# Kernel optimization log

Hardware: AMD Instinct MI355X
Metric: run time of the kernel (lower is better)

Reference implementation:

```python
import jax, jax.numpy as jnp
import numpy as np

B, HH, WW, DENC = 32, 14, 14, 256
E, H, V, A, T = 512, 512, 30000, 256, 20


def setup_inputs() -> dict:
    key = jax.random.key(0)
    ks = jax.random.split(key, 16)
    s = 0.02
    return {
        "encoder_out": jax.random.normal(ks[0], (B, HH, WW, DENC), jnp.float32),
        "captions": jax.random.randint(ks[1], (B, T), 0, V),
        # Attention params (stored [in, out])
        "W_enc_att": jax.random.normal(ks[2], (DENC, A), jnp.float32) * s,
        "b_enc_att": jnp.zeros((A,), jnp.float32),
        "W_dec_att": jax.random.normal(ks[3], (H, A), jnp.float32) * s,
        "b_dec_att": jnp.zeros((A,), jnp.float32),
        "W_full": jax.random.normal(ks[4], (A, 1), jnp.float32) * s,
        "b_full": jnp.zeros((1,), jnp.float32),
        # Embedding table
        "emb": jax.random.normal(ks[5], (V, E), jnp.float32) * s,
        # LSTMCell params, torch gate order (i, f, g, o) stacked on out dim
        "W_ih": jax.random.normal(ks[6], (E + DENC, 4 * H), jnp.float32) * s,
        "b_ih": jnp.zeros((4 * H,), jnp.float32),
        "W_hh": jax.random.normal(ks[7], (H, 4 * H), jnp.float32) * s,
        "b_hh": jnp.zeros((4 * H,), jnp.float32),
        # Output projection
        "W_fc": jax.random.normal(ks[8], (H, V), jnp.float32) * s,
        "b_fc": jnp.zeros((V,), jnp.float32),
    }


def reference(encoder_out, captions, W_enc_att, b_enc_att, W_dec_att, b_dec_att,
              W_full, b_full, emb, W_ih, b_ih, W_hh, b_hh, W_fc, b_fc):
    # Flatten spatial dims: [B, P, DENC], P = HH*WW
    enc = encoder_out.reshape(encoder_out.shape[0], -1, encoder_out.shape[-1])
    # att1 is constant across timesteps (same math as recomputing each step)
    att1 = enc @ W_enc_att + b_enc_att            # [B, P, A]
    embeddings = emb[captions]                    # [B, T, E]
    x_seq = jnp.swapaxes(embeddings, 0, 1)        # [T, B, E]

    h0 = jnp.zeros((enc.shape[0], H), enc.dtype)
    c0 = jnp.zeros((enc.shape[0], H), enc.dtype)

    def step(carry, x_t):
        h, c = carry
        # Additive attention
        att2 = h @ W_dec_att + b_dec_att                          # [B, A]
        e = (jnp.tanh(att1 + att2[:, None, :]) @ W_full + b_full)[..., 0]  # [B, P]
        alpha = jax.nn.softmax(e, axis=1)                         # [B, P]
        context = jnp.einsum('bp,bpd->bd', alpha, enc)            # [B, DENC]
        # LSTMCell
        x = jnp.concatenate([x_t, context], axis=1)               # [B, E+DENC]
        gates = x @ W_ih + b_ih + h @ W_hh + b_hh                 # [B, 4H]
        i, f, g, o = jnp.split(gates, 4, axis=1)
        c_new = jax.nn.sigmoid(f) * c + jax.nn.sigmoid(i) * jnp.tanh(g)
        h_new = jax.nn.sigmoid(o) * jnp.tanh(c_new)
        # Dropout is identity in eval mode
        out = h_new @ W_fc + b_fc                                 # [B, V]
        return (h_new, c_new), out

    _, outs = jax.lax.scan(step, (h0, c0), x_seq)                 # [T, B, V]
    return jnp.swapaxes(outs, 0, 1)                               # [B, T, V]
```

## Files before the change

kernel.cpp:

```cpp
#include <hip/hip_runtime.h>
#include <hip/hip_bf16.h>
#include <cstddef>

#define BB 32
#define PP 196
#define DENC 256
#define EE 512
#define HH 512
#define AA 256
#define VV 30000
#define TT 20
#define BH (BB*HH)
#define G4 (4*HH)
#define VPAD 30080

typedef __attribute__((ext_vector_type(8))) short short8;
typedef __attribute__((ext_vector_type(4))) float f32x4;

__device__ __forceinline__ float fast_sigmoid(float x) {
    return 1.f / (1.f + __expf(-x));
}
__device__ __forceinline__ float fast_tanh(float x) {
    x = fminf(fmaxf(x, -15.f), 15.f);
    float e = __expf(2.f * x);
    return (e - 1.f) / (e + 1.f);
}
__device__ __forceinline__ void split_bf16(float x, unsigned short& hi, unsigned short& lo) {
    const unsigned u = __float_as_uint(x);
    hi = (unsigned short)(u >> 16);
    const float r = x - __uint_as_float(u & 0xffff0000u);
    lo = (unsigned short)(__float_as_uint(r) >> 16);
}

__global__ void att1_kernel(const float* __restrict__ enc,
                            const float* __restrict__ W,
                            const float* __restrict__ bias,
                            float* __restrict__ att1) {
    __shared__ float xs[8][DENC];
    const int tid = threadIdx.x;
    const int r0 = blockIdx.x * 8;
    #pragma unroll
    for (int bi = 0; bi < 8; ++bi)
        xs[bi][tid] = enc[(size_t)(r0 + bi) * DENC + tid];
    __syncthreads();
    float acc[8];
    const float bv = bias[tid];
    #pragma unroll
    for (int bi = 0; bi < 8; ++bi) acc[bi] = bv;
    #pragma unroll 8
    for (int k = 0; k < DENC; ++k) {
        const float w = W[k * AA + tid];
        #pragma unroll
        for (int bi = 0; bi < 8; ++bi) acc[bi] += xs[bi][k] * w;
    }
    #pragma unroll
    for (int bi = 0; bi < 8; ++bi)
        att1[(size_t)(r0 + bi) * AA + tid] = acc[bi];
}

__global__ void epre_kernel(const int* __restrict__ captions,
                            const float* __restrict__ emb,
                            const float* __restrict__ Wih,
                            const float* __restrict__ bih,
                            const float* __restrict__ bhh,
                            float* __restrict__ Epre) {
    __shared__ float xs[8][EE];
    const int tid = threadIdx.x;
    const int jc = blockIdx.x;
    const int mg = blockIdx.y;
    const int j = jc * 256 + tid;

    #pragma unroll
    for (int i = 0; i < 8; ++i) {
        const int m = mg * 8 + i;
        const int t = m >> 5, b = m & 31;
        const int cap = captions[b * TT + t];
        const float* erow = emb + (size_t)cap * EE;
        xs[i][tid]       = erow[tid];
        xs[i][tid + 256] = erow[tid + 256];
    }
    __syncthreads();

    float acc[8];
    const float bv = bih[j] + bhh[j];
    #pragma unroll
    for (int i = 0; i < 8; ++i) acc[i] = bv;
    #pragma unroll 8
    for (int k = 0; k < EE; ++k) {
        const float w = Wih[(size_t)k * G4 + j];
        #pragma unroll
        for (int i = 0; i < 8; ++i) acc[i] += xs[i][k] * w;
    }
    #pragma unroll
    for (int i = 0; i < 8; ++i)
        Epre[(size_t)(mg * 8 + i) * G4 + j] = acc[i];
}

__global__ __launch_bounds__(1024) void attn_step_kernel(
        int t,
        const float* __restrict__ att1,
        const float* __restrict__ enc,
        float* __restrict__ Hall,
        float* __restrict__ cbuf,
        const float* __restrict__ gates,
        float* __restrict__ context,
        const float* __restrict__ Wda,
        const float* __restrict__ bda,
        const float* __restrict__ Wfull,
        const float* __restrict__ bfull) {
    __shared__ float h_s[HH];
    __shared__ float part[4][256];
    __shared__ float att2_s[AA];
    __shared__ float e_s[256];
    __shared__ float red_s[256];
    const int b = blockIdx.x;
    const int tid = threadIdx.x;

    if (tid < 512) {
        if (t == 0) {
            h_s[tid] = 0.f;
            cbuf[b * HH + tid] = 0.f;
        } else {
            const float* g = gates + b * G4;
            const float gi = g[tid];
            const float gf = g[HH + tid];
            const float gg = g[2 * HH + tid];
            const float go = g[3 * HH + tid];
            const float cp = cbuf[b * HH + tid];
            const float cn = fast_sigmoid(gf) * cp + fast_sigmoid(gi) * fast_tanh(gg);
            const float hn = fast_sigmoid(go) * fast_tanh(cn);
            cbuf[b * HH + tid] = cn;
            Hall[(size_t)(t - 1) * BH + b * HH + tid] = hn;
            h_s[tid] = hn;
        }
    }
    __syncthreads();

    {
        const int q = tid >> 8, col = tid & 255;
        const float* W = Wda + (size_t)(q * 128) * AA + col;
        const float* hh = h_s + q * 128;
        float acc = 0.f;
        #pragma unroll 16
        for (int k = 0; k < 128; ++k) acc += hh[k] * W[(size_t)k * AA];
        part[q][col] = acc;
    }
    __syncthreads();
    if (tid < 256)
        att2_s[tid] = part[0][tid] + part[1][tid] + part[2][tid] + part[3][tid] + bda[tid];
    __syncthreads();

    {
        const int wave = tid >> 6, lane = tid & 63;
        const float bf0 = bfull[0];
        for (int p = wave; p < PP; p += 16) {
            const float* row = att1 + ((size_t)b * PP + p) * AA;
            float s = 0.f;
            #pragma unroll
            for (int q = 0; q < 4; ++q) {
                const int a = lane + q * 64;
                s += fast_tanh(row[a] + att2_s[a]) * Wfull[a];
            }
            #pragma unroll
            for (int off = 32; off > 0; off >>= 1) s += __shfl_down(s, off, 64);
            if (lane == 0) e_s[p] = s + bf0;
        }
    }
    __syncthreads();

    const float val = (tid < PP) ? e_s[tid] : -3.4e38f;
    if (tid < 256) red_s[tid] = val;
    __syncthreads();
    #pragma unroll
    for (int s = 128; s > 0; s >>= 1) {
        if (tid < s) red_s[tid] = fmaxf(red_s[tid], red_s[tid + s]);
        __syncthreads();
    }
    const float mx = red_s[0];
    __syncthreads();
    const float ex = (tid < PP) ? __expf(val - mx) : 0.f;
    if (tid < 256) red_s[tid] = ex;
    __syncthreads();
    #pragma unroll
    for (int s = 128; s > 0; s >>= 1) {
        if (tid < s) red_s[tid] += red_s[tid + s];
        __syncthreads();
    }
    const float inv = 1.f / red_s[0];
    __syncthreads();
    if (tid < 256) e_s[tid] = ex * inv;
    __syncthreads();

    {
        const int q = tid >> 8, col = tid & 255;
        const float* erow = enc + (size_t)b * PP * DENC + col;
        float acc = 0.f;
        const int p0 = q * 49;
        #pragma unroll 7
        for (int p = p0; p < p0 + 49; ++p) acc += e_s[p] * erow[(size_t)p * DENC];
        part[q][col] = acc;
    }
    __syncthreads();
    if (tid < 256)
        context[b * DENC + tid] = part[0][tid] + part[1][tid] + part[2][tid] + part[3][tid];
}

__global__ __launch_bounds__(1024) void gates_kernel(
        int t,
        const float* __restrict__ context,
        const float* __restrict__ Hall,
        const float* __restrict__ Epre,
        const float* __restrict__ Wih,
        const float* __restrict__ Whh,
        float* __restrict__ gates) {
    __shared__ float xs[4][768];
    __shared__ float part[4][256];
    const int tid = threadIdx.x;
    const int jc = blockIdx.x;
    const int bg = blockIdx.y;

    for (int idx = tid; idx < 4 * 768; idx += 1024) {
        const int bi = idx / 768;
        const int k = idx - bi * 768;
        const int b = bg * 4 + bi;
        float v;
        if (k < 256) v = context[b * DENC + k];
        else v = (t > 0) ? Hall[(size_t)(t - 1) * BH + b * HH + (k - 256)] : 0.f;
        xs[bi][k] = v;
    }
    __syncthreads();

    const int kq = tid >> 8;
    const int r = tid & 255;
    const int jl = r & 63, bl = r >> 6;
    const int j = jc * 64 + jl;
    const float* xrow = xs[bl];

    float acc = 0.f;
    if (kq == 0) {
        const float* W1 = Wih + (size_t)512 * G4 + j;
        #pragma unroll 16
        for (int k = 0; k < 192; ++k) acc += xrow[k] * W1[(size_t)k * G4];
    } else if (kq == 1) {
        const float* W1 = Wih + (size_t)704 * G4 + j;
        #pragma unroll 16
        for (int k = 0; k < 64; ++k) acc += xrow[192 + k] * W1[(size_t)k * G4];
        const float* W2 = Whh + j;
        #pragma unroll 16
        for (int k = 0; k < 128; ++k) acc += xrow[256 + k] * W2[(size_t)k * G4];
    } else if (kq == 2) {
        const float* W2 = Whh + (size_t)128 * G4 + j;
        #pragma unroll 16
        for (int k = 0; k < 192; ++k) acc += xrow[384 + k] * W2[(size_t)k * G4];
    } else {
        const float* W2 = Whh + (size_t)320 * G4 + j;
        #pragma unroll 16
        for (int k = 0; k < 192; ++k) acc += xrow[576 + k] * W2[(size_t)k * G4];
    }
    part[kq][r] = acc;
    __syncthreads();

    if (tid < 256) {
        const int b = bg * 4 + bl;
        gates[(size_t)b * G4 + j] = part[0][tid] + part[1][tid] + part[2][tid] + part[3][tid]
                                  + Epre[(size_t)(t * BB + b) * G4 + j];
    }
}

__global__ void final_update_kernel(const float* __restrict__ gates,
                                    const float* __restrict__ cbuf,
                                    float* __restrict__ Hall) {
    const int idx = blockIdx.x * 256 + threadIdx.x;
    const int b = idx >> 9, hi = idx & 511;
    const float* g = gates + b * G4;
    const float gi = g[hi];
    const float gf = g[HH + hi];
    const float gg = g[2 * HH + hi];
    const float go = g[3 * HH + hi];
    const float cp = cbuf[idx];
    const float cn = fast_sigmoid(gf) * cp + fast_sigmoid(gi) * fast_tanh(gg);
    const float hn = fast_sigmoid(go) * fast_tanh(cn);
    Hall[(size_t)(TT - 1) * BH + idx] = hn;
}

__global__ void split_hall_kernel(const float* __restrict__ Hall,
                                  unsigned short* __restrict__ Ah,
                                  unsigned short* __restrict__ Al) {
    const int idx = blockIdx.x * 256 + threadIdx.x;
    unsigned short h, l;
    split_bf16(Hall[idx], h, l);
    Ah[idx] = h; Al[idx] = l;
}

__global__ void split_wfc_kernel(const float* __restrict__ Wfc,
                                 unsigned short* __restrict__ Wt_h,
                                 unsigned short* __restrict__ Wt_l) {
    __shared__ unsigned short th[64][66];
    __shared__ unsigned short tl[64][66];
    const int tid = threadIdx.x;
    const int k0 = blockIdx.x * 64;
    const int v0 = blockIdx.y * 64;

    const int c = tid & 63, r0 = tid >> 6;
    #pragma unroll
    for (int i = 0; i < 16; ++i) {
        const int r = r0 + i * 4;
        const int v = v0 + c;
        const float x = (v < VV) ? Wfc[(size_t)(k0 + r) * VV + v] : 0.f;
        unsigned short h, l;
        split_bf16(x, h, l);
        th[r][c] = h; tl[r][c] = l;
    }
    __syncthreads();

    const int v = tid >> 2, q = tid & 3;
    short8 oh0, oh1, ol0, ol1;
    #pragma unroll
    for (int i = 0; i < 8; ++i) {
        oh0[i] = (short)th[q * 16 + i][v];
        oh1[i] = (short)th[q * 16 + 8 + i][v];
        ol0[i] = (short)tl[q * 16 + i][v];
        ol1[i] = (short)tl[q * 16 + 8 + i][v];
    }
    unsigned short* dh = Wt_h + (size_t)(v0 + v) * HH + k0 + q * 16;
    unsigned short* dl = Wt_l + (size_t)(v0 + v) * HH + k0 + q * 16;
    *(short8*)(dh) = oh0; *(short8*)(dh + 8) = oh1;
    *(short8*)(dl) = ol0; *(short8*)(dl + 8) = ol1;
}

#define LDK 40

__global__ __launch_bounds__(256) void gemm_out_mfma_pre(
        const unsigned short* __restrict__ Ah,
        const unsigned short* __restrict__ Al,
        const unsigned short* __restrict__ Wt_h,
        const unsigned short* __restrict__ Wt_l,
        const float* __restrict__ bfc,
        float* __restrict__ out) {
    __shared__ unsigned short As_h[128 * LDK];
    __shared__ unsigned short As_l[128 * LDK];
    __shared__ unsigned short Bs_h[128 * LDK];
    __shared__ unsigned short Bs_l[128 * LDK];

    const int tid = threadIdx.x;
    const int m0 = blockIdx.x * 128;
    const int v0 = blockIdx.y * 128;

    const int wave = tid >> 6, lane = tid & 63;
    const int wm = wave & 1, wn = wave >> 1;
    const int row16 = lane & 15, quad = lane >> 4;

    const int sn = tid & 127;
    const int skq = tid >> 7;

    f32x4 acc[4][4] = {};

    #pragma unroll 1
    for (int k0 = 0; k0 < HH; k0 += 32) {
        {
            const size_t src = (size_t)(m0 + sn) * HH + k0 + skq * 16;
            const short8 h0 = *(const short8*)(Ah + src);
            const short8 h1 = *(const short8*)(Ah + src + 8);
            const short8 l0 = *(const short8*)(Al + src);
            const short8 l1 = *(const short8*)(Al + src + 8);
            unsigned short* dh = &As_h[sn * LDK + skq * 16];
            unsigned short* dl = &As_l[sn * LDK + skq * 16];
            *(short8*)(dh) = h0; *(short8*)(dh + 8) = h1;
            *(short8*)(dl) = l0; *(short8*)(dl + 8) = l1;
        }
        {
            const size_t src = (size_t)(v0 + sn) * HH + k0 + skq * 16;
            const short8 h0 = *(const short8*)(Wt_h + src);
            const short8 h1 = *(const short8*)(Wt_h + src + 8);
            const short8 l0 = *(const short8*)(Wt_l + src);
            const short8 l1 = *(const short8*)(Wt_l + src + 8);
            unsigned short* dh = &Bs_h[sn * LDK + skq * 16];
            unsigned short* dl = &Bs_l[sn * LDK + skq * 16];
            *(short8*)(dh) = h0; *(short8*)(dh + 8) = h1;
            *(short8*)(dl) = l0; *(short8*)(dl + 8) = l1;
        }
        __syncthreads();

        short8 ah[4], al[4], bh[4], bl[4];
        #pragma unroll
        for (int mi = 0; mi < 4; ++mi) {
            const int off = (wm * 64 + mi * 16 + row16) * LDK + quad * 8;
            ah[mi] = *(const short8*)&As_h[off];
            al[mi] = *(const short8*)&As_l[off];
        }
        #pragma unroll
        for (int ni = 0; ni < 4; ++ni) {
            const int off = (wn * 64 + ni * 16 + row16) * LDK + quad * 8;
            bh[ni] = *(const short8*)&Bs_h[off];
            bl[ni] = *(const short8*)&Bs_l[off];
        }
        #pragma unroll
        for (int mi = 0; mi < 4; ++mi) {
            #pragma unroll
            for (int ni = 0; ni < 4; ++ni) {
                acc[mi][ni] = __builtin_amdgcn_mfma_f32_16x16x32_bf16(
                    ah[mi], bh[ni], acc[mi][ni], 0, 0, 0);
                acc[mi][ni] = __builtin_amdgcn_mfma_f32_16x16x32_bf16(
                    ah[mi], bl[ni], acc[mi][ni], 0, 0, 0);
                acc[mi][ni] = __builtin_amdgcn_mfma_f32_16x16x32_bf16(
                    al[mi], bh[ni], acc[mi][ni], 0, 0, 0);
            }
        }
        __syncthreads();
    }

    #pragma unroll
    for (int ni = 0; ni < 4; ++ni) {
        const int v = v0 + wn * 64 + ni * 16 + row16;
        if (v >= VV) continue;
        const float bias = bfc[v];
        #pragma unroll
        for (int mi = 0; mi < 4; ++mi) {
            const int mbase = m0 + wm * 64 + mi * 16 + quad * 4;
            #pragma unroll
            for (int r = 0; r < 4; ++r) {
                const int m = mbase + r;
                const int t_idx = m >> 5;
                const int b_idx = m & 31;
                out[((size_t)b_idx * TT + t_idx) * VV + v] = acc[mi][ni][r] + bias;
            }
        }
    }
}

__global__ __launch_bounds__(256) void gemm_out_mfma_fb(
        const float* __restrict__ Hall,
        const float* __restrict__ Wfc,
        const float* __restrict__ bfc,
        float* __restrict__ out) {
    __shared__ unsigned short As_h[128 * LDK];
    __shared__ unsigned short As_l[128 * LDK];
    __shared__ unsigned short Bs_h[128 * LDK];
    __shared__ unsigned short Bs_l[128 * LDK];

    const int tid = threadIdx.x;
    const int m0 = blockIdx.x * 128;
    const int v0 = blockIdx.y * 128;

    const int wave = tid >> 6, lane = tid & 63;
    const int wm = wave & 1, wn = wave >> 1;
    const int row16 = lane & 15, quad = lane >> 4;

    const int sn = tid & 127;
    const int skq = tid >> 7;

    f32x4 acc[4][4] = {};

    #pragma unroll 1
    for (int k0 = 0; k0 < HH; k0 += 32) {
        {
            const float* asrc = Hall + (size_t)(m0 + sn) * HH + k0 + skq * 16;
            short8 h0, h1, l0, l1;
            #pragma unroll
            for (int i = 0; i < 16; i += 4) {
                const float4 v = *reinterpret_cast<const float4*>(asrc + i);
                const float vv[4] = {v.x, v.y, v.z, v.w};
                #pragma unroll
                for (int jj = 0; jj < 4; ++jj) {
                    unsigned short hb, lb;
                    split_bf16(vv[jj], hb, lb);
                    const int e = i + jj;
                    if (e < 8) { h0[e] = (short)hb; l0[e] = (short)lb; }
                    else       { h1[e - 8] = (short)hb; l1[e - 8] = (short)lb; }
                }
            }
            unsigned short* dh = &As_h[sn * LDK + skq * 16];
            unsigned short* dl = &As_l[sn * LDK + skq * 16];
            *(short8*)(dh) = h0; *(short8*)(dh + 8) = h1;
            *(short8*)(dl) = l0; *(short8*)(dl + 8) = l1;
        }
        {
            const int vcol = v0 + sn;
            const bool ok = vcol < VV;
            const float* bsrc = Wfc + (size_t)(k0 + skq * 16) * VV + vcol;
            short8 h0, h1, l0, l1;
            #pragma unroll
            for (int i = 0; i < 16; ++i) {
                const float x = ok ? bsrc[(size_t)i * VV] : 0.f;
                unsigned short hb, lb;
                split_bf16(x, hb, lb);
                if (i < 8) { h0[i] = (short)hb; l0[i] = (short)lb; }
                else       { h1[i - 8] = (short)hb; l1[i - 8] = (short)lb; }
            }
            unsigned short* dh = &Bs_h[sn * LDK + skq * 16];
            unsigned short* dl = &Bs_l[sn * LDK + skq * 16];
            *(short8*)(dh) = h0; *(short8*)(dh + 8) = h1;
            *(short8*)(dl) = l0; *(short8*)(dl + 8) = l1;
        }
        __syncthreads();

        short8 ah[4], al[4], bh[4], bl[4];
        #pragma unroll
        for (int mi = 0; mi < 4; ++mi) {
            const int off = (wm * 64 + mi * 16 + row16) * LDK + quad * 8;
            ah[mi] = *(const short8*)&As_h[off];
            al[mi] = *(const short8*)&As_l[off];
        }
        #pragma unroll
        for (int ni = 0; ni < 4; ++ni) {
            const int off = (wn * 64 + ni * 16 + row16) * LDK + quad * 8;
            bh[ni] = *(const short8*)&Bs_h[off];
            bl[ni] = *(const short8*)&Bs_l[off];
        }
        #pragma unroll
        for (int mi = 0; mi < 4; ++mi) {
            #pragma unroll
            for (int ni = 0; ni < 4; ++ni) {
                acc[mi][ni] = __builtin_amdgcn_mfma_f32_16x16x32_bf16(
                    ah[mi], bh[ni], acc[mi][ni], 0, 0, 0);
                acc[mi][ni] = __builtin_amdgcn_mfma_f32_16x16x32_bf16(
                    ah[mi], bl[ni], acc[mi][ni], 0, 0, 0);
                acc[mi][ni] = __builtin_amdgcn_mfma_f32_16x16x32_bf16(
                    al[mi], bh[ni], acc[mi][ni], 0, 0, 0);
            }
        }
        __syncthreads();
    }

    #pragma unroll
    for (int ni = 0; ni < 4; ++ni) {
        const int v = v0 + wn * 64 + ni * 16 + row16;
        if (v >= VV) continue;
        const float bias = bfc[v];
        #pragma unroll
        for (int mi = 0; mi < 4; ++mi) {
            const int mbase = m0 + wm * 64 + mi * 16 + quad * 4;
            #pragma unroll
            for (int r = 0; r < 4; ++r) {
                const int m = mbase + r;
                const int t_idx = m >> 5;
                const int b_idx = m & 31;
                out[((size_t)b_idx * TT + t_idx) * VV + v] = acc[mi][ni][r] + bias;
            }
        }
    }
}

extern "C" void kernel_launch(void* const* d_in, const int* in_sizes, int n_in,
                              void* d_out, int out_size, void* d_ws, size_t ws_size,
                              hipStream_t stream) {
    const float* enc      = (const float*)d_in[0];
    const int*   captions = (const int*)  d_in[1];
    const float* Wea      = (const float*)d_in[2];
    const float* bea      = (const float*)d_in[3];
    const float* Wda      = (const float*)d_in[4];
    const float* bda      = (const float*)d_in[5];
    const float* Wfull    = (const float*)d_in[6];
    const float* bfull    = (const float*)d_in[7];
    const float* emb      = (const float*)d_in[8];
    const float* Wih      = (const float*)d_in[9];
    const float* bih      = (const float*)d_in[10];
    const float* Whh      = (const float*)d_in[11];
    const float* bhh      = (const float*)d_in[12];
    const float* Wfc      = (const float*)d_in[13];
    const float* bfc      = (const float*)d_in[14];
    float* out = (float*)d_out;

    float* ws      = (float*)d_ws;
    float* att1    = ws;
    float* Hall    = att1 + 1605632;
    float* cbuf    = Hall + 327680;
    float* context = cbuf + 16384;
    float* gates   = context + 8192;
    float* Epre    = gates + 65536;
    float* tail    = Epre + 1310720;
    unsigned short* Ah   = (unsigned short*)tail;
    unsigned short* Al   = Ah + 640 * 512;
    unsigned short* Wt_h = Al + 640 * 512;
    unsigned short* Wt_l = Wt_h + (size_t)VPAD * HH;
    const size_t need_bytes =
        (size_t)(3334144) * 4 +
        (size_t)(2 * 640 * 512) * 2 +
        (size_t)(2 * (size_t)VPAD * HH) * 2;
    const bool pre = ws_size >= need_bytes;

    att1_kernel<<<dim3(784), dim3(256), 0, stream>>>(enc, Wea, bea, att1);
    epre_kernel<<<dim3(8, 80), dim3(256), 0, stream>>>(captions, emb, Wih, bih, bhh, Epre);
    if (pre) {
        split_wfc_kernel<<<dim3(8, VPAD / 64), dim3(256), 0, stream>>>(Wfc, Wt_h, Wt_l);
    }

    for (int t = 0; t < TT; ++t) {
        attn_step_kernel<<<dim3(BB), dim3(1024), 0, stream>>>(
            t, att1, enc, Hall, cbuf, gates, context, Wda, bda, Wfull, bfull);
        gates_kernel<<<dim3(32, 8), dim3(1024), 0, stream>>>(
            t, context, Hall, Epre, Wih, Whh, gates);
    }
    final_update_kernel<<<dim3(64), dim3(256), 0, stream>>>(gates, cbuf, Hall);

    if (pre) {
        split_hall_kernel<<<dim3(1280), dim3(256), 0, stream>>>(Hall, Ah, Al);
        gemm_out_mfma_pre<<<dim3(5, 235), dim3(256), 0, stream>>>(
            Ah, Al, Wt_h, Wt_l, bfc, out);
    } else {
        gemm_out_mfma_fb<<<dim3(5, 235), dim3(256), 0, stream>>>(Hall, Wfc, bfc, out);
    }
}
```

Before: 1.028 ms.

## Fuse recurrent timestep loop into one cooperative persistent kernel with grid barriers

The 41 per-timestep launches (attention, gates and final update kernels) are replaced by one cooperative kernel of 256 blocks. Each block keeps its LSTM cell state in a register, and an atomic-counter grid barrier separates the attention and gate phases of every step. The bf16 hi/lo split of the hidden state is written inside the loop, so the separate split kernel is no longer needed. This removes launch overhead and the global round-trips of the gate and cell buffers, but adds spin-barrier latency and relies on all 256 blocks being co-resident. If the cooperative launch fails, the old multi-kernel path runs instead.

Result: slower. 2.914 ms (+183.6%).

```diff
diff --git a/kernel.cpp b/kernel.cpp
--- a/kernel.cpp
+++ b/kernel.cpp
@@ -1,5 +1,4 @@
 #include <hip/hip_runtime.h>
-#include <hip/hip_bf16.h>
 #include <cstddef>
 
 #define BB 32
@@ -13,6 +12,7 @@
 #define BH (BB*HH)
 #define G4 (4*HH)
 #define VPAD 30080
+#define NBLK 256
 
 typedef __attribute__((ext_vector_type(8))) short short8;
 typedef __attribute__((ext_vector_type(4))) float f32x4;
@@ -32,10 +32,25 @@
     lo = (unsigned short)(__float_as_uint(r) >> 16);
 }
 
+__device__ __forceinline__ void grid_barrier(unsigned* bar, unsigned target) {
+    __syncthreads();
+    if (threadIdx.x == 0) {
+        __threadfence();
+        __hip_atomic_fetch_add(bar, 1u, __ATOMIC_RELEASE, __HIP_MEMORY_SCOPE_AGENT);
+        while (__hip_atomic_load(bar, __ATOMIC_ACQUIRE, __HIP_MEMORY_SCOPE_AGENT) < target) {
+            __builtin_amdgcn_s_sleep(1);
+        }
+        __threadfence();
+    }
+    __syncthreads();
+}
+
 __global__ void att1_kernel(const float* __restrict__ enc,
                             const float* __restrict__ W,
                             const float* __restrict__ bias,
-                            float* __restrict__ att1) {
+                            float* __restrict__ att1,
+                            unsigned* __restrict__ bar) {
+    if (blockIdx.x == 0 && threadIdx.x == 0) *bar = 0;
     __shared__ float xs[8][DENC];
     const int tid = threadIdx.x;
     const int r0 = blockIdx.x * 8;
@@ -94,6 +109,194 @@
     #pragma unroll
     for (int i = 0; i < 8; ++i)
         Epre[(size_t)(mg * 8 + i) * G4 + j] = acc[i];
+}
+
+__global__ __launch_bounds__(1024) void fused_loop_kernel(
+        const float* __restrict__ att1,
+        const float* __restrict__ enc,
+        const float* __restrict__ Wda,
+        const float* __restrict__ bda,
+        const float* __restrict__ Wfull,
+        const float* __restrict__ bfull,
+        const float* __restrict__ Wih,
+        const float* __restrict__ Whh,
+        const float* __restrict__ Epre,
+        float* __restrict__ hbuf,
+        float* __restrict__ ctxb,
+        float* __restrict__ Hall,
+        unsigned short* __restrict__ Ah,
+        unsigned short* __restrict__ Al,
+        unsigned* bar,
+        int write_split) {
+    const int bid = blockIdx.x;
+    const int tid = threadIdx.x;
+    const int jc = bid & 31;
+    const int bg = bid >> 5;
+
+    __shared__ float h_s[HH];
+    __shared__ float part[4][256];
+    __shared__ float att2_s[AA];
+    __shared__ float e_s[256];
+    __shared__ float red_s[256];
+    __shared__ float xs[4][768];
+    __shared__ float gred[256];
+
+    unsigned bar_target = 0;
+    float c_reg = 0.f;
+
+    if (bid < 32 && tid < 512) hbuf[16384 + bid * HH + tid] = 0.f;
+
+    for (int t = 0; t < TT; ++t) {
+        const float* hprev = hbuf + ((t + 1) & 1) * 16384;
+
+        if (bid < 32) {
+            const int b = bid;
+            if (tid < 512) h_s[tid] = hprev[b * HH + tid];
+            __syncthreads();
+            {
+                const int q = tid >> 8, col = tid & 255;
+                const float* W = Wda + (size_t)(q * 128) * AA + col;
+                const float* hh = h_s + q * 128;
+                float acc = 0.f;
+                #pragma unroll 16
+                for (int k = 0; k < 128; ++k) acc += hh[k] * W[(size_t)k * AA];
+                part[q][col] = acc;
+            }
+            __syncthreads();
+            if (tid < 256)
+                att2_s[tid] = part[0][tid] + part[1][tid] + part[2][tid] + part[3][tid] + bda[tid];
+            __syncthreads();
+            {
+                const int wave = tid >> 6, lane = tid & 63;
+                const float bf0 = bfull[0];
+                for (int p = wave; p < PP; p += 16) {
+                    const float* row = att1 + ((size_t)b * PP + p) * AA;
+                    float s = 0.f;
+                    #pragma unroll
+                    for (int q = 0; q < 4; ++q) {
+                        const int a = lane + q * 64;
+                        s += fast_tanh(row[a] + att2_s[a]) * Wfull[a];
+                    }
+                    #pragma unroll
+                    for (int off = 32; off > 0; off >>= 1) s += __shfl_down(s, off, 64);
+                    if (lane == 0) e_s[p] = s + bf0;
+                }
+            }
+            __syncthreads();
+            const float val = (tid < PP) ? e_s[tid] : -3.4e38f;
+            if (tid < 256) red_s[tid] = val;
+            __syncthreads();
+            #pragma unroll
+            for (int s = 128; s > 0; s >>= 1) {
+                if (tid < s) red_s[tid] = fmaxf(red_s[tid], red_s[tid + s]);
+                __syncthreads();
+            }
+            const float mx = red_s[0];
+            __syncthreads();
+            const float ex = (tid < PP) ? __expf(val - mx) : 0.f;
+            if (tid < 256) red_s[tid] = ex;
+            __syncthreads();
+            #pragma unroll
+            for (int s = 128; s > 0; s >>= 1) {
+                if (tid < s) red_s[tid] += red_s[tid + s];
+                __syncthreads();
+            }
+            const float inv = 1.f / red_s[0];
+            __syncthreads();
+            if (tid < 256) e_s[tid] = ex * inv;
+            __syncthreads();
+            {
+                const int q = tid >> 8, col = tid & 255;
+                const float* erow = enc + (size_t)b * PP * DENC + col;
+                float acc = 0.f;
+                const int p0 = q * 49;
+                #pragma unroll 7
+                for (int p = p0; p < p0 + 49; ++p) acc += e_s[p] * erow[(size_t)p * DENC];
+                part[q][col] = acc;
+            }
+            __syncthreads();
+            if (tid < 256)
+                ctxb[b * DENC + tid] = part[0][tid] + part[1][tid] + part[2][tid] + part[3][tid];
+        }
+        bar_target += NBLK;
+        grid_barrier(bar, bar_target);
+
+        #pragma unroll
+        for (int ii = 0; ii < 3; ++ii) {
+            const int idx = tid + ii * 1024;
+            const int bi = idx / 768;
+            const int k = idx - bi * 768;
+            const int b = bg * 4 + bi;
+            xs[bi][k] = (k < 256) ? ctxb[b * DENC + k] : hprev[b * HH + (k - 256)];
+        }
+        __syncthreads();
+        {
+            const int kq = tid >> 8;
+            const int r = tid & 255;
+            const int bl = r >> 6;
+            const int cl = r & 63;
+            const int col = ((cl >> 4) * 512) + jc * 16 + (cl & 15);
+            const float* xrow = xs[bl];
+            float acc = 0.f;
+            if (kq == 0) {
+                const float* W1 = Wih + (size_t)512 * G4 + col;
+                #pragma unroll 16
+                for (int k = 0; k < 192; ++k) acc += xrow[k] * W1[(size_t)k * G4];
+            } else if (kq == 1) {
+                const float* W1 = Wih + (size_t)704 * G4 + col;
+                #pragma unroll 16
+                for (int k = 0; k < 64; ++k) acc += xrow[192 + k] * W1[(size_t)k * G4];
+                const float* W2 = Whh + col;
+                #pragma unroll 16
+                for (int k = 0; k < 128; ++k) acc += xrow[256 + k] * W2[(size_t)k * G4];
+            } else if (kq == 2) {
+                const float* W2 = Whh + (size_t)128 * G4 + col;
+                #pragma unroll 16
+                for (int k = 0; k < 192; ++k) acc += xrow[384 + k] * W2[(size_t)k * G4];
+            } else {
+                const float* W2 = Whh + (size_t)320 * G4 + col;
+                #pragma unroll 16
+                for (int k = 0; k < 192; ++k) acc += xrow[576 + k] * W2[(size_t)k * G4];
+            }
+            part[kq][r] = acc;
+        }
+        __syncthreads();
+        if (tid < 256) {
+            const int bl = tid >> 6;
+            const int cl = tid & 63;
+            const int b = bg * 4 + bl;
+            const int col = ((cl >> 4) * 512) + jc * 16 + (cl & 15);
+            gred[tid] = part[0][tid] + part[1][tid] + part[2][tid] + part[3][tid]
+                      + Epre[(size_t)(t * BB + b) * G4 + col];
+        }
+        __syncthreads();
+        if (tid < 64) {
+            const int bl = tid >> 4;
+            const int hdl = tid & 15;
+            const float gi = gred[bl * 64 +  0 + hdl];
+            const float gf = gred[bl * 64 + 16 + hdl];
+            const float gg = gred[bl * 64 + 32 + hdl];
+            const float go = gred[bl * 64 + 48 + hdl];
+            const float cn = fast_sigmoid(gf) * c_reg + fast_sigmoid(gi) * fast_tanh(gg);
+            const float hn = fast_sigmoid(go) * fast_tanh(cn);
+            c_reg = cn;
+            const int b = bg * 4 + bl;
+            const int hd = jc * 16 + hdl;
+            hbuf[(t & 1) * 16384 + b * HH + hd] = hn;
+            const size_t mi = (size_t)(t * BB + b) * HH + hd;
+            Hall[mi] = hn;
+            if (write_split) {
+                unsigned short hh_, ll_;
+                split_bf16(hn, hh_, ll_);
+                Ah[mi] = hh_;
+                Al[mi] = ll_;
+            }
+        }
+        if (t < TT - 1) {
+            bar_target += NBLK;
+            grid_barrier(bar, bar_target);
+        }
+    }
 }
 
 __global__ __launch_bounds__(1024) void attn_step_kernel(
@@ -561,40 +764,55 @@
     const float* bfc      = (const float*)d_in[14];
     float* out = (float*)d_out;
 
-    float* ws      = (float*)d_ws;
-    float* att1    = ws;
-    float* Hall    = att1 + 1605632;
-    float* cbuf    = Hall + 327680;
-    float* context = cbuf + 16384;
-    float* gates   = context + 8192;
-    float* Epre    = gates + 65536;
-    float* tail    = Epre + 1310720;
+    float* ws   = (float*)d_ws;
+    float* att1 = ws;
+    float* Hall = att1 + 1605632;
+    float* Epre = Hall + 327680;
+    float* hbuf = Epre + 1310720;
+    float* ctxb = hbuf + 32768;
+    unsigned* bar = (unsigned*)(ctxb + 8192);
+    float* tail = ctxb + 8192 + 64;
     unsigned short* Ah   = (unsigned short*)tail;
     unsigned short* Al   = Ah + 640 * 512;
     unsigned short* Wt_h = Al + 640 * 512;
     unsigned short* Wt_l = Wt_h + (size_t)VPAD * HH;
     const size_t need_bytes =
-        (size_t)(3334144) * 4 +
+        (size_t)(3285056) * 4 +
         (size_t)(2 * 640 * 512) * 2 +
         (size_t)(2 * (size_t)VPAD * HH) * 2;
     const bool pre = ws_size >= need_bytes;
 
-    att1_kernel<<<dim3(784), dim3(256), 0, stream>>>(enc, Wea, bea, att1);
+    att1_kernel<<<dim3(784), dim3(256), 0, stream>>>(enc, Wea, bea, att1, bar);
     epre_kernel<<<dim3(8, 80), dim3(256), 0, stream>>>(captions, emb, Wih, bih, bhh, Epre);
     if (pre) {
         split_wfc_kernel<<<dim3(8, VPAD / 64), dim3(256), 0, stream>>>(Wfc, Wt_h, Wt_l);
     }
 
-    for (int t = 0; t < TT; ++t) {
-        attn_step_kernel<<<dim3(BB), dim3(1024), 0, stream>>>(
-            t, att1, enc, Hall, cbuf, gates, context, Wda, bda, Wfull, bfull);
-        gates_kernel<<<dim3(32, 8), dim3(1024), 0, stream>>>(
-            t, context, Hall, Epre, Wih, Whh, gates);
-    }
-    final_update_kernel<<<dim3(64), dim3(256), 0, stream>>>(gates, cbuf, Hall);
+    int write_split = pre ? 1 : 0;
+    void* cargs[] = {
+        (void*)&att1, (void*)&enc, (void*)&Wda, (void*)&bda, (void*)&Wfull, (void*)&bfull,
+        (void*)&Wih, (void*)&Whh, (void*)&Epre, (void*)&hbuf, (void*)&ctxb, (void*)&Hall,
+        (void*)&Ah, (void*)&Al, (void*)&bar, (void*)&write_split };
+    hipError_t cerr = hipLaunchCooperativeKernel(fused_loop_kernel,
+                                                 dim3(NBLK), dim3(1024),
+                                                 cargs, 0, stream);
+    if (cerr != hipSuccess) {
+        float* cbuf    = (float*)tail;
+        float* context = cbuf + 16384;
+        float* gates   = context + 8192;
+        for (int t = 0; t < TT; ++t) {
+            attn_step_kernel<<<dim3(BB), dim3(1024), 0, stream>>>(
+                t, att1, enc, Hall, cbuf, gates, context, Wda, bda, Wfull, bfull);
+            gates_kernel<<<dim3(32, 8), dim3(1024), 0, stream>>>(
+                t, context, Hall, Epre, Wih, Whh, gates);
+        }
+        final_update_kernel<<<dim3(64), dim3(256), 0, stream>>>(gates, cbuf, Hall);
+        if (pre) {
+            split_hall_kernel<<<dim3(1280), dim3(256), 0, stream>>>(Hall, Ah, Al);
+        }
+    }
 
     if (pre) {
-        split_hall_kernel<<<dim3(1280), dim3(256), 0, stream>>>(Hall, Ah, Al);
         gemm_out_mfma_pre<<<dim3(5, 235), dim3(256), 0, stream>>>(
             Ah, Al, Wt_h, Wt_l, bfc, out);
     } else {
```
